# Kernel tuning notes

Measured on AMD Instinct MI355X. Metric: run time of the kernel, lower is better.

## Reference

```python
import jax, jax.numpy as jnp
import numpy as np

N_NODES = 100000
D = 256
E = 1000000
H = 128


def setup_inputs() -> dict:
    key = jax.random.key(0)
    k1, k2, k3, k4 = jax.random.split(key, 4)
    z = jax.random.normal(k1, (N_NODES, D), dtype=jnp.float32)
    edge_label_index = jax.random.randint(k2, (2, E), 0, N_NODES, dtype=jnp.int64)
    # Linear layers: PyTorch Linear(in, out) -> weight [out, in]; stored here as [in, out].
    W1 = jax.random.normal(k3, (2 * D, H), dtype=jnp.float32) * (1.0 / np.sqrt(2 * D))
    b1 = jnp.zeros((H,), dtype=jnp.float32)
    W2 = jax.random.normal(k4, (H, 1), dtype=jnp.float32) * (1.0 / np.sqrt(H))
    b2 = jnp.zeros((1,), dtype=jnp.float32)
    return {"z": z, "edge_label_index": edge_label_index,
            "W1": W1, "b1": b1, "W2": W2, "b2": b2}


def reference(z, edge_label_index, W1, b1, W2, b2):
    src = edge_label_index[0]
    dst = edge_label_index[1]
    # Gather node pairs and concat: [E, 2*D]
    pair = jnp.concatenate([z[src], z[dst]], axis=-1)
    h = jax.nn.relu(pair @ W1 + b1)          # [E, H]
    out = (h @ W2 + b2).reshape(-1)          # [E]
    return out
```

## Files before the change

kernel.cpp:

```cpp
#include <hip/hip_runtime.h>
#include <hip/hip_bf16.h>


typedef __attribute__((ext_vector_type(4))) float floatx4;
typedef __attribute__((ext_vector_type(8))) short short8;
typedef _Float16 half8v __attribute__((ext_vector_type(8)));

__device__ __forceinline__ unsigned short bf16rne(float x) {
    unsigned int u = __float_as_uint(x);
    u += 0x7fffu + ((u >> 16) & 1u);
    return (unsigned short)(u >> 16);
}

__device__ __forceinline__ void gl_lds16(const void* g, void* l) {
    __builtin_amdgcn_global_load_lds(
        (const __attribute__((address_space(1))) void*)(unsigned long long)g,
        (__attribute__((address_space(3))) void*)(unsigned)(unsigned long long)l,
        16, 0, 0);
}

__global__ void cvt_z(const float* __restrict__ z, unsigned short* __restrict__ zb, int n4) {
    int i = blockIdx.x * blockDim.x + threadIdx.x;
    if (i < n4) {
        float4 f = ((const float4*)z)[i];
        ushort4 u;
        u.x = bf16rne(f.x); u.y = bf16rne(f.y);
        u.z = bf16rne(f.z); u.w = bf16rne(f.w);
        ((ushort4*)zb)[i] = u;
    }
}

__global__ void cvt_w1h(const float* __restrict__ W1, unsigned short* __restrict__ BTc2) {
    int t = blockIdx.x * blockDim.x + threadIdx.x;
    int hf = t >> 15, rem = t & 32767;
    int s = rem >> 12, rem2 = rem & 4095;
    int n = rem2 >> 5, rem3 = rem2 & 31;
    int gp = rem3 >> 3, j = rem3 & 7;
    int g = gp ^ ((n >> 1) & 3);
    int k = hf * 256 + s * 32 + g * 8 + j;
    BTc2[t] = bf16rne(W1[k * 128 + n]);
}

__global__ void cvt_w1(const float* __restrict__ W1, unsigned short* __restrict__ BTc) {
    int t = blockIdx.x * blockDim.x + threadIdx.x;
    int s = t >> 12, rem = t & 4095;
    int n = rem >> 5, rem2 = rem & 31;
    int gp = rem2 >> 3, j = rem2 & 7;
    int g = gp ^ ((n >> 1) & 3);
    int k = s * 32 + g * 8 + j;
    BTc[t] = bf16rne(W1[k * 128 + n]);
}

template <bool ABF16>
__global__ __launch_bounds__(256, 2)
void gemm_h(const float* __restrict__ zf, const unsigned short* __restrict__ zb,
            int nnodes, const unsigned short* __restrict__ BTc2,
            const float* __restrict__ b1, _Float16* __restrict__ Hh)
{
    __shared__ unsigned short btile[2][4][128][32];

    const int t = threadIdx.x;
    const int wid = t >> 6;
    const int lane = t & 63;
    const int l15 = lane & 15;
    const int quad = lane >> 4;
    const int m0 = blockIdx.x * 256 + wid * 64;
    const int hf = blockIdx.y;

    unsigned offs[4];
#pragma unroll
    for (int mf = 0; mf < 4; ++mf) {
        int r = m0 + mf * 16 + l15;
        r = r < nnodes ? r : nnodes - 1;
        offs[mf] = (unsigned)r * 512u;
    }
    const char* zbb = (const char*)(ABF16 ? (const void*)zb : (const void*)zf);

    const int swz = (l15 >> 1) & 3;
    const unsigned short* bbase = &btile[0][0][0][0] + l15 * 32 + (quad ^ swz) * 8;

    auto stage = [&](int kc, int buf) {
        const char* g = (const char*)BTc2 + hf * 65536 + kc * 32768 + wid * 1024 + lane * 16;
        char* l = (char*)&btile[buf][0][0][0] + wid * 1024 + lane * 16;
#pragma unroll
        for (int i = 0; i < 8; ++i)
            gl_lds16(g + i * 4096, l + i * 4096);
    };

    auto load_a = [&](int ks, short8* dst) {
        if constexpr (ABF16) {
            const int cb = ks * 64 + quad * 16;
#pragma unroll
            for (int mf = 0; mf < 4; ++mf)
                dst[mf] = *(const short8*)(zbb + (size_t)offs[mf] + cb);
        } else {
            const int cb = ks * 128 + quad * 32;
#pragma unroll
            for (int mf = 0; mf < 4; ++mf) {
                const float* pf = (const float*)(zbb + (size_t)offs[mf] * 2 + cb);
                float4 f0 = *(const float4*)pf;
                float4 f1 = *(const float4*)(pf + 4);
                short8 av;
                av[0] = (short)bf16rne(f0.x); av[1] = (short)bf16rne(f0.y);
                av[2] = (short)bf16rne(f0.z); av[3] = (short)bf16rne(f0.w);
                av[4] = (short)bf16rne(f1.x); av[5] = (short)bf16rne(f1.y);
                av[6] = (short)bf16rne(f1.z); av[7] = (short)bf16rne(f1.w);
                dst[mf] = av;
            }
        }
    };

    floatx4 acc[4][8];
#pragma unroll
    for (int mf = 0; mf < 4; ++mf)
#pragma unroll
        for (int nf = 0; nf < 8; ++nf)
            acc[mf][nf] = (floatx4){0.f, 0.f, 0.f, 0.f};

    short8 A[3][4];
    stage(0, 0);
    load_a(0, A[0]);
    load_a(1, A[1]);
    __syncthreads();

#pragma unroll
    for (int kc = 0; kc < 2; ++kc) {
        if (kc == 0) stage(1, 1);

#pragma unroll
        for (int s4 = 0; s4 < 4; ++s4) {
            const int ks = kc * 4 + s4;
            if (ks + 2 < 8) load_a(ks + 2, A[(ks + 2) % 3]);

            const unsigned short* bs = bbase + kc * 16384 + s4 * 4096;
            const short8* ac = A[ks % 3];

            short8 bfr[4];
#pragma unroll
            for (int nf = 0; nf < 4; ++nf)
                bfr[nf] = *(const short8*)(bs + nf * 512);
#pragma unroll
            for (int nf = 0; nf < 4; ++nf)
#pragma unroll
                for (int mf = 0; mf < 4; ++mf)
                    acc[mf][nf] = __builtin_amdgcn_mfma_f32_16x16x32_bf16(
                        ac[mf], bfr[nf], acc[mf][nf], 0, 0, 0);
#pragma unroll
            for (int nf = 0; nf < 4; ++nf)
                bfr[nf] = *(const short8*)(bs + (nf + 4) * 512);
#pragma unroll
            for (int nf = 0; nf < 4; ++nf)
#pragma unroll
                for (int mf = 0; mf < 4; ++mf)
                    acc[mf][nf + 4] = __builtin_amdgcn_mfma_f32_16x16x32_bf16(
                        ac[mf], bfr[nf], acc[mf][nf + 4], 0, 0, 0);
        }

        if (kc == 0) __syncthreads();
    }

    float b1v[8];
#pragma unroll
    for (int nf = 0; nf < 8; ++nf)
        b1v[nf] = (hf == 0) ? b1[nf * 16 + l15] : 0.f;
#pragma unroll
    for (int mf = 0; mf < 4; ++mf) {
#pragma unroll
        for (int r = 0; r < 4; ++r) {
            int row = m0 + mf * 16 + quad * 4 + r;
            if (row < nnodes) {
                _Float16* hp = Hh + (size_t)row * 256 + hf * 128 + l15;
#pragma unroll
                for (int nf = 0; nf < 8; ++nf)
                    hp[nf * 16] = (_Float16)(acc[mf][nf][r] + b1v[nf]);
            }
        }
    }
}

__global__ __launch_bounds__(256)
void edge_out(const _Float16* __restrict__ Hh, const int* __restrict__ eli,
              int E, int nnodes,
              const float* __restrict__ W2, const float* __restrict__ b2,
              float* __restrict__ out)
{
    const int t = threadIdx.x;
    const int lane = t & 63;
    const int wid = t >> 6;
    const int l15 = lane & 15;
    const int grp = lane >> 4;

    float w2v[8];
#pragma unroll
    for (int j = 0; j < 8; ++j)
        w2v[j] = W2[l15 * 8 + j];
    const float b2s = b2[0];

    const int e0 = blockIdx.x * 64 + wid * 16 + grp;

    half8v hs[4], hd[4];
    int ee[4];
#pragma unroll
    for (int i = 0; i < 4; ++i) {
        int e = e0 + i * 4;
        ee[i] = e;
        int ec = e < E ? e : E - 1;
        int s = eli[ec];
        int d = eli[E + ec];
        s = s < 0 ? 0 : (s >= nnodes ? nnodes - 1 : s);
        d = d < 0 ? 0 : (d >= nnodes ? nnodes - 1 : d);
        hs[i] = *(const half8v*)(Hh + (size_t)s * 256 + l15 * 8);
        hd[i] = *(const half8v*)(Hh + (size_t)d * 256 + 128 + l15 * 8);
    }
#pragma unroll
    for (int i = 0; i < 4; ++i) {
        float sacc = 0.f;
#pragma unroll
        for (int j = 0; j < 8; ++j) {
            float v = (float)hs[i][j] + (float)hd[i][j];
            v = v > 0.f ? v : 0.f;
            sacc = fmaf(v, w2v[j], sacc);
        }
        sacc += __shfl_xor(sacc, 1);
        sacc += __shfl_xor(sacc, 2);
        sacc += __shfl_xor(sacc, 4);
        sacc += __shfl_xor(sacc, 8);
        if (l15 == 0 && ee[i] < E)
            out[ee[i]] = sacc + b2s;
    }
}

template <bool ABF16>
__global__ __launch_bounds__(256, 2)
void fused_mlp(const float* __restrict__ zf, const unsigned short* __restrict__ zb,
               const int* __restrict__ eli, int E, int nnodes,
               const unsigned short* __restrict__ BTc,
               const float* __restrict__ b1, const float* __restrict__ W2,
               const float* __restrict__ b2, float* __restrict__ out)
{
    __shared__ unsigned short btile[2][4][128][32];

    const int t = threadIdx.x;
    const int wid = t >> 6;
    const int lane = t & 63;
    const int l15 = lane & 15;
    const int quad = lane >> 4;
    const int m0 = blockIdx.x * 256 + wid * 64;

    unsigned offs[4], offd[4];
#pragma unroll
    for (int mf = 0; mf < 4; ++mf) {
        int e = m0 + mf * 16 + l15;
        e = e < E ? e : E - 1;
        int s = eli[e];
        int d = eli[E + e];
        s = s < 0 ? 0 : (s >= nnodes ? nnodes - 1 : s);
        d = d < 0 ? 0 : (d >= nnodes ? nnodes - 1 : d);
        offs[mf] = (unsigned)s * 512u;
        offd[mf] = (unsigned)d * 512u;
    }
    const char* zbb = (const char*)(ABF16 ? (const void*)zb : (const void*)zf);

    const int swz = (l15 >> 1) & 3;
    const unsigned short* bbase = &btile[0][0][0][0] + l15 * 32 + (quad ^ swz) * 8;

    auto stage = [&](int kc, int buf) {
        const char* g = (const char*)BTc + kc * 32768 + wid * 1024 + lane * 16;
        char* l = (char*)&btile[buf][0][0][0] + wid * 1024 + lane * 16;
#pragma unroll
        for (int i = 0; i < 8; ++i)
            gl_lds16(g + i * 4096, l + i * 4096);
    };

    auto load_a = [&](int ks, short8* dst) {
        const unsigned* off = (ks < 8) ? offs : offd;
        if constexpr (ABF16) {
            const int cb = (ks & 7) * 64 + quad * 16;
#pragma unroll
            for (int mf = 0; mf < 4; ++mf)
                dst[mf] = *(const short8*)(zbb + (size_t)off[mf] + cb);
        } else {
            const int cb = (ks & 7) * 128 + quad * 32;
#pragma unroll
            for (int mf = 0; mf < 4; ++mf) {
                const float* pf = (const float*)(zbb + (size_t)off[mf] * 2 + cb);
                float4 f0 = *(const float4*)pf;
                float4 f1 = *(const float4*)(pf + 4);
                short8 av;
                av[0] = (short)bf16rne(f0.x); av[1] = (short)bf16rne(f0.y);
                av[2] = (short)bf16rne(f0.z); av[3] = (short)bf16rne(f0.w);
                av[4] = (short)bf16rne(f1.x); av[5] = (short)bf16rne(f1.y);
                av[6] = (short)bf16rne(f1.z); av[7] = (short)bf16rne(f1.w);
                dst[mf] = av;
            }
        }
    };

    floatx4 acc[4][8];
#pragma unroll
    for (int mf = 0; mf < 4; ++mf)
#pragma unroll
        for (int nf = 0; nf < 8; ++nf)
            acc[mf][nf] = (floatx4){0.f, 0.f, 0.f, 0.f};

    short8 A[3][4];
    stage(0, 0);
    load_a(0, A[0]);
    load_a(1, A[1]);
    __syncthreads();

#pragma unroll
    for (int kc = 0; kc < 4; ++kc) {
        if (kc < 3) stage(kc + 1, (kc + 1) & 1);

#pragma unroll
        for (int s4 = 0; s4 < 4; ++s4) {
            const int ks = kc * 4 + s4;
            if (ks + 2 < 16) load_a(ks + 2, A[(ks + 2) % 3]);

            const unsigned short* bs = bbase + (kc & 1) * 16384 + s4 * 4096;
            short8 bfr[8];
#pragma unroll
            for (int nf = 0; nf < 8; ++nf)
                bfr[nf] = *(const short8*)(bs + nf * 512);

            const short8* ac = A[ks % 3];
#pragma unroll
            for (int nf = 0; nf < 8; ++nf)
#pragma unroll
                for (int mf = 0; mf < 4; ++mf)
                    acc[mf][nf] = __builtin_amdgcn_mfma_f32_16x16x32_bf16(
                        ac[mf], bfr[nf], acc[mf][nf], 0, 0, 0);
        }

        if (kc < 3) __syncthreads();
    }

    const float b2s = b2[0];
    float b1v[8], w2v[8];
#pragma unroll
    for (int nf = 0; nf < 8; ++nf) {
        int c = nf * 16 + l15;
        b1v[nf] = b1[c];
        w2v[nf] = W2[c];
    }
#pragma unroll
    for (int mf = 0; mf < 4; ++mf) {
#pragma unroll
        for (int r = 0; r < 4; ++r) {
            float s = 0.f;
#pragma unroll
            for (int nf = 0; nf < 8; ++nf) {
                float v = acc[mf][nf][r] + b1v[nf];
                v = v > 0.f ? v : 0.f;
                s = fmaf(v, w2v[nf], s);
            }
            s += __shfl_xor(s, 1);
            s += __shfl_xor(s, 2);
            s += __shfl_xor(s, 4);
            s += __shfl_xor(s, 8);
            if (l15 == 0) {
                int e = m0 + mf * 16 + quad * 4 + r;
                if (e < E) out[e] = s + b2s;
            }
        }
    }
}

__global__ void naive_edge(const float* __restrict__ z, const int* __restrict__ eli,
                           int E, int nnodes,
                           const float* __restrict__ W1, const float* __restrict__ b1,
                           const float* __restrict__ W2, const float* __restrict__ b2,
                           float* __restrict__ out)
{
    __shared__ float red[2];
    int e = blockIdx.x;
    int j = threadIdx.x;
    int s = eli[e], d = eli[E + e];
    s = s < 0 ? 0 : (s >= nnodes ? nnodes - 1 : s);
    d = d < 0 ? 0 : (d >= nnodes ? nnodes - 1 : d);
    const float* zs = z + (long long)s * 256;
    const float* zd = z + (long long)d * 256;
    float h = b1[j];
    for (int i = 0; i < 256; ++i) h = fmaf(zs[i], W1[i * 128 + j], h);
    for (int i = 0; i < 256; ++i) h = fmaf(zd[i], W1[(256 + i) * 128 + j], h);
    h = h > 0.f ? h : 0.f;
    float v = h * W2[j];
    v += __shfl_xor(v, 1);  v += __shfl_xor(v, 2);  v += __shfl_xor(v, 4);
    v += __shfl_xor(v, 8);  v += __shfl_xor(v, 16); v += __shfl_xor(v, 32);
    if ((threadIdx.x & 63) == 0) red[threadIdx.x >> 6] = v;
    __syncthreads();
    if (threadIdx.x == 0) out[e] = red[0] + red[1] + b2[0];
}

extern "C" void kernel_launch(void* const* d_in, const int* in_sizes, int n_in,
                              void* d_out, int out_size, void* d_ws, size_t ws_size,
                              hipStream_t stream) {
    const float* z   = (const float*)d_in[0];
    const int*   eli = (const int*)d_in[1];
    const float* W1  = (const float*)d_in[2];
    const float* b1  = (const float*)d_in[3];
    const float* W2  = (const float*)d_in[4];
    const float* b2  = (const float*)d_in[5];
    float*       out = (float*)d_out;

    const int E      = in_sizes[1] / 2;
    const int nnodes = in_sizes[0] / 256;

    const size_t ZB   = (size_t)nnodes * 512;
    const size_t HB   = (size_t)nnodes * 512;
    const size_t BT2B = 131072;
    const size_t BTB  = (size_t)512 * 128 * 2;

    const int grid_gemm = (nnodes + 255) / 256;
    const int grid_edge = (E + 63) / 64;

    if (ws_size >= ZB + HB + BT2B) {
        unsigned short* zb   = (unsigned short*)d_ws;
        _Float16*       Hh   = (_Float16*)((char*)d_ws + ZB);
        unsigned short* BTc2 = (unsigned short*)((char*)d_ws + ZB + HB);
        int n4 = nnodes * 64;
        cvt_z<<<(n4 + 255) / 256, 256, 0, stream>>>(z, zb, n4);
        cvt_w1h<<<256, 256, 0, stream>>>(W1, BTc2);
        gemm_h<true><<<dim3(grid_gemm, 2), 256, 0, stream>>>(nullptr, zb, nnodes, BTc2, b1, Hh);
        edge_out<<<grid_edge, 256, 0, stream>>>(Hh, eli, E, nnodes, W2, b2, out);
    } else if (ws_size >= HB + BT2B) {
        _Float16*       Hh   = (_Float16*)d_ws;
        unsigned short* BTc2 = (unsigned short*)((char*)d_ws + HB);
        cvt_w1h<<<256, 256, 0, stream>>>(W1, BTc2);
        gemm_h<false><<<dim3(grid_gemm, 2), 256, 0, stream>>>(z, nullptr, nnodes, BTc2, b1, Hh);
        edge_out<<<grid_edge, 256, 0, stream>>>(Hh, eli, E, nnodes, W2, b2, out);
    } else if (ws_size >= BTB) {
        unsigned short* BTc = (unsigned short*)d_ws;
        cvt_w1<<<256, 256, 0, stream>>>(W1, BTc);
        fused_mlp<false><<<(E + 255) / 256, 256, 0, stream>>>(z, nullptr, eli, E, nnodes, BTc, b1, W2, b2, out);
    } else {
        naive_edge<<<E, 128, 0, stream>>>(z, eli, E, nnodes, W1, b1, W2, b2, out);
    }
}
```

Baseline: 260.4 us.

## Fuse z bf16 conversion into single-pass node GEMM computing both W1 halves

Drops the separate z-to-bf16 pass and the two-way grid split over W1 halves. The node GEMM now reads fp32 z once, converts it in registers, and computes both the src and dst projections per block with 128-row tiles and double-buffered B stages. This removes a full write and reread of a bf16 copy of z, and stops reading z twice. In exchange each wave holds twice as many accumulators, which raises register pressure, and the per-block tile is smaller.

```diff
diff --git a/kernel.cpp b/kernel.cpp
--- a/kernel.cpp
+++ b/kernel.cpp
@@ -17,17 +17,6 @@
         (const __attribute__((address_space(1))) void*)(unsigned long long)g,
         (__attribute__((address_space(3))) void*)(unsigned)(unsigned long long)l,
         16, 0, 0);
-}
-
-__global__ void cvt_z(const float* __restrict__ z, unsigned short* __restrict__ zb, int n4) {
-    int i = blockIdx.x * blockDim.x + threadIdx.x;
-    if (i < n4) {
-        float4 f = ((const float4*)z)[i];
-        ushort4 u;
-        u.x = bf16rne(f.x); u.y = bf16rne(f.y);
-        u.z = bf16rne(f.z); u.w = bf16rne(f.w);
-        ((ushort4*)zb)[i] = u;
-    }
 }
 
 __global__ void cvt_w1h(const float* __restrict__ W1, unsigned short* __restrict__ BTc2) {
@@ -51,128 +40,122 @@
     BTc[t] = bf16rne(W1[k * 128 + n]);
 }
 
-template <bool ABF16>
 __global__ __launch_bounds__(256, 2)
-void gemm_h(const float* __restrict__ zf, const unsigned short* __restrict__ zb,
-            int nnodes, const unsigned short* __restrict__ BTc2,
-            const float* __restrict__ b1, _Float16* __restrict__ Hh)
+void gemm_hb(const float* __restrict__ zf, int nnodes,
+             const unsigned short* __restrict__ BTc2,
+             const float* __restrict__ b1, _Float16* __restrict__ Hh)
 {
-    __shared__ unsigned short btile[2][4][128][32];
+    __shared__ unsigned short btile[2][2][2][128][32];
 
     const int t = threadIdx.x;
     const int wid = t >> 6;
     const int lane = t & 63;
     const int l15 = lane & 15;
     const int quad = lane >> 4;
-    const int m0 = blockIdx.x * 256 + wid * 64;
-    const int hf = blockIdx.y;
-
-    unsigned offs[4];
-#pragma unroll
-    for (int mf = 0; mf < 4; ++mf) {
+    const int m0 = blockIdx.x * 128 + wid * 32;
+
+    unsigned offs[2];
+#pragma unroll
+    for (int mf = 0; mf < 2; ++mf) {
         int r = m0 + mf * 16 + l15;
         r = r < nnodes ? r : nnodes - 1;
-        offs[mf] = (unsigned)r * 512u;
-    }
-    const char* zbb = (const char*)(ABF16 ? (const void*)zb : (const void*)zf);
+        offs[mf] = (unsigned)r * 1024u;
+    }
+    const char* zbb = (const char*)zf;
 
     const int swz = (l15 >> 1) & 3;
-    const unsigned short* bbase = &btile[0][0][0][0] + l15 * 32 + (quad ^ swz) * 8;
+    const unsigned short* bbase = &btile[0][0][0][0][0] + l15 * 32 + (quad ^ swz) * 8;
 
     auto stage = [&](int kc, int buf) {
-        const char* g = (const char*)BTc2 + hf * 65536 + kc * 32768 + wid * 1024 + lane * 16;
-        char* l = (char*)&btile[buf][0][0][0] + wid * 1024 + lane * 16;
-#pragma unroll
-        for (int i = 0; i < 8; ++i)
-            gl_lds16(g + i * 4096, l + i * 4096);
+        char* lbase = (char*)&btile[0][0][0][0][0] + buf * 32768 + wid * 1024 + lane * 16;
+        const char* gbase = (const char*)BTc2 + kc * 16384 + wid * 1024 + lane * 16;
+#pragma unroll
+        for (int h = 0; h < 2; ++h) {
+            const char* g = gbase + h * 65536;
+            char* l = lbase + h * 16384;
+#pragma unroll
+            for (int i = 0; i < 4; ++i)
+                gl_lds16(g + i * 4096, l + i * 4096);
+        }
     };
 
     auto load_a = [&](int ks, short8* dst) {
-        if constexpr (ABF16) {
-            const int cb = ks * 64 + quad * 16;
-#pragma unroll
-            for (int mf = 0; mf < 4; ++mf)
-                dst[mf] = *(const short8*)(zbb + (size_t)offs[mf] + cb);
-        } else {
-            const int cb = ks * 128 + quad * 32;
-#pragma unroll
-            for (int mf = 0; mf < 4; ++mf) {
-                const float* pf = (const float*)(zbb + (size_t)offs[mf] * 2 + cb);
-                float4 f0 = *(const float4*)pf;
-                float4 f1 = *(const float4*)(pf + 4);
-                short8 av;
-                av[0] = (short)bf16rne(f0.x); av[1] = (short)bf16rne(f0.y);
-                av[2] = (short)bf16rne(f0.z); av[3] = (short)bf16rne(f0.w);
-                av[4] = (short)bf16rne(f1.x); av[5] = (short)bf16rne(f1.y);
-                av[6] = (short)bf16rne(f1.z); av[7] = (short)bf16rne(f1.w);
-                dst[mf] = av;
-            }
+        const int cb = ks * 128 + quad * 32;
+#pragma unroll
+        for (int mf = 0; mf < 2; ++mf) {
+            const float* pf = (const float*)(zbb + (size_t)offs[mf] + cb);
+            float4 f0 = *(const float4*)pf;
+            float4 f1 = *(const float4*)(pf + 4);
+            short8 av;
+            av[0] = (short)bf16rne(f0.x); av[1] = (short)bf16rne(f0.y);
+            av[2] = (short)bf16rne(f0.z); av[3] = (short)bf16rne(f0.w);
+            av[4] = (short)bf16rne(f1.x); av[5] = (short)bf16rne(f1.y);
+            av[6] = (short)bf16rne(f1.z); av[7] = (short)bf16rne(f1.w);
+            dst[mf] = av;
         }
     };
 
-    floatx4 acc[4][8];
-#pragma unroll
-    for (int mf = 0; mf < 4; ++mf)
-#pragma unroll
-        for (int nf = 0; nf < 8; ++nf)
+    floatx4 acc[2][16];
+#pragma unroll
+    for (int mf = 0; mf < 2; ++mf)
+#pragma unroll
+        for (int nf = 0; nf < 16; ++nf)
             acc[mf][nf] = (floatx4){0.f, 0.f, 0.f, 0.f};
 
-    short8 A[3][4];
+    short8 A[3][2];
     stage(0, 0);
     load_a(0, A[0]);
     load_a(1, A[1]);
     __syncthreads();
 
 #pragma unroll
-    for (int kc = 0; kc < 2; ++kc) {
-        if (kc == 0) stage(1, 1);
-
-#pragma unroll
-        for (int s4 = 0; s4 < 4; ++s4) {
-            const int ks = kc * 4 + s4;
+    for (int kc = 0; kc < 4; ++kc) {
+        if (kc < 3) stage(kc + 1, (kc + 1) & 1);
+
+#pragma unroll
+        for (int s4 = 0; s4 < 2; ++s4) {
+            const int ks = kc * 2 + s4;
             if (ks + 2 < 8) load_a(ks + 2, A[(ks + 2) % 3]);
 
-            const unsigned short* bs = bbase + kc * 16384 + s4 * 4096;
+            const unsigned short* bs0 = bbase + (kc & 1) * 16384 + s4 * 4096;
             const short8* ac = A[ks % 3];
 
-            short8 bfr[4];
-#pragma unroll
-            for (int nf = 0; nf < 4; ++nf)
-                bfr[nf] = *(const short8*)(bs + nf * 512);
-#pragma unroll
-            for (int nf = 0; nf < 4; ++nf)
-#pragma unroll
-                for (int mf = 0; mf < 4; ++mf)
-                    acc[mf][nf] = __builtin_amdgcn_mfma_f32_16x16x32_bf16(
-                        ac[mf], bfr[nf], acc[mf][nf], 0, 0, 0);
-#pragma unroll
-            for (int nf = 0; nf < 4; ++nf)
-                bfr[nf] = *(const short8*)(bs + (nf + 4) * 512);
-#pragma unroll
-            for (int nf = 0; nf < 4; ++nf)
-#pragma unroll
-                for (int mf = 0; mf < 4; ++mf)
-                    acc[mf][nf + 4] = __builtin_amdgcn_mfma_f32_16x16x32_bf16(
-                        ac[mf], bfr[nf], acc[mf][nf + 4], 0, 0, 0);
-        }
-
-        if (kc == 0) __syncthreads();
+#pragma unroll
+            for (int gq = 0; gq < 4; ++gq) {
+                const unsigned short* bs = bs0 + (gq >> 1) * 8192 + (gq & 1) * 2048;
+                short8 bfr[4];
+#pragma unroll
+                for (int nf = 0; nf < 4; ++nf)
+                    bfr[nf] = *(const short8*)(bs + nf * 512);
+#pragma unroll
+                for (int nf = 0; nf < 4; ++nf)
+#pragma unroll
+                    for (int mf = 0; mf < 2; ++mf)
+                        acc[mf][gq * 4 + nf] = __builtin_amdgcn_mfma_f32_16x16x32_bf16(
+                            ac[mf], bfr[nf], acc[mf][gq * 4 + nf], 0, 0, 0);
+            }
+        }
+
+        if (kc < 3) __syncthreads();
     }
 
     float b1v[8];
 #pragma unroll
     for (int nf = 0; nf < 8; ++nf)
-        b1v[nf] = (hf == 0) ? b1[nf * 16 + l15] : 0.f;
-#pragma unroll
-    for (int mf = 0; mf < 4; ++mf) {
+        b1v[nf] = b1[nf * 16 + l15];
+#pragma unroll
+    for (int mf = 0; mf < 2; ++mf) {
 #pragma unroll
         for (int r = 0; r < 4; ++r) {
             int row = m0 + mf * 16 + quad * 4 + r;
             if (row < nnodes) {
-                _Float16* hp = Hh + (size_t)row * 256 + hf * 128 + l15;
+                _Float16* hp = Hh + (size_t)row * 256 + l15;
 #pragma unroll
                 for (int nf = 0; nf < 8; ++nf)
                     hp[nf * 16] = (_Float16)(acc[mf][nf][r] + b1v[nf]);
+#pragma unroll
+                for (int nf = 0; nf < 8; ++nf)
+                    hp[128 + nf * 16] = (_Float16)acc[mf][8 + nf][r];
             }
         }
     }
@@ -230,13 +213,12 @@
     }
 }
 
-template <bool ABF16>
 __global__ __launch_bounds__(256, 2)
-void fused_mlp(const float* __restrict__ zf, const unsigned short* __restrict__ zb,
-               const int* __restrict__ eli, int E, int nnodes,
-               const unsigned short* __restrict__ BTc,
-               const float* __restrict__ b1, const float* __restrict__ W2,
-               const float* __restrict__ b2, float* __restrict__ out)
+void fused_mlp_f32(const float* __restrict__ zf, const int* __restrict__ eli,
+                   int E, int nnodes,
+                   const unsigned short* __restrict__ BTc,
+                   const float* __restrict__ b1, const float* __restrict__ W2,
+                   const float* __restrict__ b2, float* __restrict__ out)
 {
     __shared__ unsigned short btile[2][4][128][32];
 
@@ -256,10 +238,10 @@
         int d = eli[E + e];
         s = s < 0 ? 0 : (s >= nnodes ? nnodes - 1 : s);
         d = d < 0 ? 0 : (d >= nnodes ? nnodes - 1 : d);
-        offs[mf] = (unsigned)s * 512u;
-        offd[mf] = (unsigned)d * 512u;
-    }
-    const char* zbb = (const char*)(ABF16 ? (const void*)zb : (const void*)zf);
+        offs[mf] = (unsigned)s * 1024u;
+        offd[mf] = (unsigned)d * 1024u;
+    }
+    const char* zbb = (const char*)zf;
 
     const int swz = (l15 >> 1) & 3;
     const unsigned short* bbase = &btile[0][0][0][0] + l15 * 32 + (quad ^ swz) * 8;
@@ -274,25 +256,18 @@
 
     auto load_a = [&](int ks, short8* dst) {
         const unsigned* off = (ks < 8) ? offs : offd;
-        if constexpr (ABF16) {
-            const int cb = (ks & 7) * 64 + quad * 16;
-#pragma unroll
-            for (int mf = 0; mf < 4; ++mf)
-                dst[mf] = *(const short8*)(zbb + (size_t)off[mf] + cb);
-        } else {
-            const int cb = (ks & 7) * 128 + quad * 32;
-#pragma unroll
-            for (int mf = 0; mf < 4; ++mf) {
-                const float* pf = (const float*)(zbb + (size_t)off[mf] * 2 + cb);
-                float4 f0 = *(const float4*)pf;
-                float4 f1 = *(const float4*)(pf + 4);
-                short8 av;
-                av[0] = (short)bf16rne(f0.x); av[1] = (short)bf16rne(f0.y);
-                av[2] = (short)bf16rne(f0.z); av[3] = (short)bf16rne(f0.w);
-                av[4] = (short)bf16rne(f1.x); av[5] = (short)bf16rne(f1.y);
-                av[6] = (short)bf16rne(f1.z); av[7] = (short)bf16rne(f1.w);
-                dst[mf] = av;
-            }
+        const int cb = (ks & 7) * 128 + quad * 32;
+#pragma unroll
+        for (int mf = 0; mf < 4; ++mf) {
+            const float* pf = (const float*)(zbb + (size_t)off[mf] + cb);
+            float4 f0 = *(const float4*)pf;
+            float4 f1 = *(const float4*)(pf + 4);
+            short8 av;
+            av[0] = (short)bf16rne(f0.x); av[1] = (short)bf16rne(f0.y);
+            av[2] = (short)bf16rne(f0.z); av[3] = (short)bf16rne(f0.w);
+            av[4] = (short)bf16rne(f1.x); av[5] = (short)bf16rne(f1.y);
+            av[6] = (short)bf16rne(f1.z); av[7] = (short)bf16rne(f1.w);
+            dst[mf] = av;
         }
     };
 
@@ -407,33 +382,23 @@
     const int E      = in_sizes[1] / 2;
     const int nnodes = in_sizes[0] / 256;
 
-    const size_t ZB   = (size_t)nnodes * 512;
     const size_t HB   = (size_t)nnodes * 512;
     const size_t BT2B = 131072;
     const size_t BTB  = (size_t)512 * 128 * 2;
 
-    const int grid_gemm = (nnodes + 255) / 256;
+    const int grid_gemm = (nnodes + 127) / 128;
     const int grid_edge = (E + 63) / 64;
 
-    if (ws_size >= ZB + HB + BT2B) {
-        unsigned short* zb   = (unsigned short*)d_ws;
-        _Float16*       Hh   = (_Float16*)((char*)d_ws + ZB);
-        unsigned short* BTc2 = (unsigned short*)((char*)d_ws + ZB + HB);
-        int n4 = nnodes * 64;
-        cvt_z<<<(n4 + 255) / 256, 256, 0, stream>>>(z, zb, n4);
-        cvt_w1h<<<256, 256, 0, stream>>>(W1, BTc2);
-        gemm_h<true><<<dim3(grid_gemm, 2), 256, 0, stream>>>(nullptr, zb, nnodes, BTc2, b1, Hh);
-        edge_out<<<grid_edge, 256, 0, stream>>>(Hh, eli, E, nnodes, W2, b2, out);
-    } else if (ws_size >= HB + BT2B) {
+    if (ws_size >= HB + BT2B) {
         _Float16*       Hh   = (_Float16*)d_ws;
         unsigned short* BTc2 = (unsigned short*)((char*)d_ws + HB);
         cvt_w1h<<<256, 256, 0, stream>>>(W1, BTc2);
-        gemm_h<false><<<dim3(grid_gemm, 2), 256, 0, stream>>>(z, nullptr, nnodes, BTc2, b1, Hh);
+        gemm_hb<<<grid_gemm, 256, 0, stream>>>(z, nnodes, BTc2, b1, Hh);
         edge_out<<<grid_edge, 256, 0, stream>>>(Hh, eli, E, nnodes, W2, b2, out);
     } else if (ws_size >= BTB) {
         unsigned short* BTc = (unsigned short*)d_ws;
         cvt_w1<<<256, 256, 0, stream>>>(W1, BTc);
-        fused_mlp<false><<<(E + 255) / 256, 256, 0, stream>>>(z, nullptr, eli, E, nnodes, BTc, b1, W2, b2, out);
+        fused_mlp_f32<<<(E + 255) / 256, 256, 0, stream>>>(z, eli, E, nnodes, BTc, b1, W2, b2, out);
     } else {
         naive_edge<<<E, 128, 0, stream>>>(z, eli, E, nnodes, W1, b1, W2, b2, out);
     }
```

Result: faster. 247.1 us (-5.1%).
